# Optimization experiments

Measured on AMD Instinct MI355X. Metric: run time of the kernel, lower is better.

## Reference

```python
import jax, jax.numpy as jnp
import numpy as np

S, B, D, H = 2048, 2, 1024, 16
DK = D // H


def _rope_tables(seq_len, dk):
    inv_freq = 1.0 / (10000.0 ** (np.arange(0, dk, 2, dtype=np.float32) / dk))
    ang = np.arange(seq_len, dtype=np.float32)[:, None] * inv_freq[None, :]  # [S, dk/2]
    ang = np.concatenate([ang, ang], axis=-1)  # [S, dk]
    cos = jnp.asarray(np.cos(ang))[None, None]  # [1,1,S,dk]
    sin = jnp.asarray(np.sin(ang))[None, None]
    return cos, sin


def rotate_half(x):
    x1, x2 = x[..., : x.shape[-1] // 2], x[..., x.shape[-1] // 2 :]
    return jnp.concatenate([-x2, x1], axis=-1)


def apply_rope(x, cos, sin):
    return x * cos + rotate_half(x) * sin


def setup_inputs() -> dict:
    key = jax.random.key(0)
    ks = jax.random.split(key, 12)
    Q = jax.random.normal(ks[0], (S, B, D), dtype=jnp.float32)
    K = jax.random.normal(ks[1], (S, B, D), dtype=jnp.float32)
    V = jax.random.normal(ks[2], (S, B, D), dtype=jnp.float32)
    s = 0.02
    W_q = jax.random.normal(ks[3], (D, D), dtype=jnp.float32) * s
    W_k = jax.random.normal(ks[4], (D, D), dtype=jnp.float32) * s
    W_v = jax.random.normal(ks[5], (D, D), dtype=jnp.float32) * s
    W_o = jax.random.normal(ks[6], (D, D), dtype=jnp.float32) * s
    b_q = jnp.zeros((D,), jnp.float32)
    b_k = jnp.zeros((D,), jnp.float32)
    b_v = jnp.zeros((D,), jnp.float32)
    b_o = jnp.zeros((D,), jnp.float32)
    cos, sin = _rope_tables(S, DK)
    mask = jnp.triu(jnp.ones((S, S), dtype=bool), k=1)[None, None]  # causal, True = masked
    return {
        "Q": Q, "K": K, "V": V,
        "W_q": W_q, "b_q": b_q, "W_k": W_k, "b_k": b_k,
        "W_v": W_v, "b_v": b_v, "W_o": W_o, "b_o": b_o,
        "q_rotary_cos": cos, "q_rotary_sin": sin,
        "k_rotary_cos": cos, "k_rotary_sin": sin,
        "mask": mask,
    }


def reference(Q, K, V, W_q, b_q, W_k, b_k, W_v, b_v, W_o, b_o,
              q_rotary_cos, q_rotary_sin, k_rotary_cos, k_rotary_sin, mask):
    q_len, bsz, _ = Q.shape
    # [S,B,D] -> [S,B,H,dk] -> [B,H,S,dk]
    def proj(x, W, b):
        y = x @ W.T + b
        return y.reshape(x.shape[0], bsz, H, DK).transpose(1, 2, 0, 3)
    q_s = apply_rope(proj(Q, W_q, b_q), q_rotary_cos, q_rotary_sin)
    k_s = apply_rope(proj(K, W_k, b_k), k_rotary_cos, k_rotary_sin)
    v_s = proj(V, W_v, b_v)
    scores = jnp.einsum("bhqd,bhkd->bhqk", q_s, k_s) / jnp.sqrt(jnp.float32(DK))
    scores = jnp.where(mask, jnp.float32(-1e9), scores)
    attn = jax.nn.softmax(scores, axis=-1)
    context = jnp.einsum("bhqk,bhkd->bhqd", attn, v_s)  # [B,H,S,dk]
    context = context.transpose(2, 0, 1, 3).reshape(q_len, bsz, D)
    return context @ W_o.T + b_o
```

## Files before the change

### kernel.cpp

```cpp
#include <hip/hip_runtime.h>
#include <cstdint>
#include <cstddef>

typedef __bf16 bf16;
typedef __bf16 bf16x2 __attribute__((ext_vector_type(2)));
typedef __bf16 bf16x4 __attribute__((ext_vector_type(4)));
typedef __bf16 bf16x8 __attribute__((ext_vector_type(8)));
typedef float f32x4 __attribute__((ext_vector_type(4)));

#define S_LEN 2048
#define BATCH 2
#define DM 1024
#define NH 16
#define DKH 64
#define MTOT (S_LEN * BATCH)

__device__ __forceinline__ void gload_lds16(const void* g, void* l) {
    __builtin_amdgcn_global_load_lds((const __attribute__((address_space(1))) uint32_t*)g,
                                     (__attribute__((address_space(3))) uint32_t*)l, 16, 0, 0);
}

__device__ __forceinline__ uint32_t pack2(float a, float b) {
    bf16x2 v; v[0] = (bf16)a; v[1] = (bf16)b;
    return __builtin_bit_cast(uint32_t, v);
}

struct ConvArgs { const float* src[7]; bf16* dst[7]; };

__global__ __launch_bounds__(256) void convert_all(ConvArgs a) {
    int gid = blockIdx.x * 256 + threadIdx.x;
    int tid, off;
    if (gid < 3 * 524288) { tid = gid >> 19; off = gid & 524287; }
    else { int r = gid - 3 * 524288; tid = 3 + (r >> 17); off = r & 131071; }
    const float4* s4 = (const float4*)a.src[tid];
    float4 x = s4[2 * off], y = s4[2 * off + 1];
    bf16x8 v;
    v[0] = (bf16)x.x; v[1] = (bf16)x.y; v[2] = (bf16)x.z; v[3] = (bf16)x.w;
    v[4] = (bf16)y.x; v[5] = (bf16)y.y; v[6] = (bf16)y.z; v[7] = (bf16)y.w;
    *(bf16x8*)(a.dst[tid] + 8 * (size_t)off) = v;
}

template<int MI>
__device__ __forceinline__ void gemm_core(const bf16* __restrict__ A, const bf16* __restrict__ Bt,
                                          const float* __restrict__ bias, void* __restrict__ out,
                                          int mode, const float* __restrict__ cosp,
                                          const float* __restrict__ sinp, bf16* As, bf16* Bs) {
    constexpr int TN = (MI == 4) ? 128 : 64;
    constexpr int BH = (TN == 128) ? 4096 : 2048;
    const int K = DM;
    int t = threadIdx.x;
    int lane = t & 63, wave = t >> 6;
    int lm = lane & 15, quad = lane >> 4;
    int m0 = blockIdx.y * 128, n0 = blockIdx.x * TN;
    int wm, wn;
    if constexpr (MI == 4) { wm = (wave >> 1) * 64; wn = (wave & 1) * 64; }
    else { wm = wave * 32; wn = 0; }
    f32x4 acc[MI][4] = {};
    int rowg = t >> 2, kc = (t & 3) * 8;
    const bf16* agp0 = A + (size_t)(m0 + rowg) * K + kc;
    const bf16* agp1 = A + (size_t)(m0 + 64 + rowg) * K + kc;
    const bf16* bgp0 = Bt + (size_t)(n0 + rowg) * K + kc;
    const bf16* bgp1 = (TN == 128) ? Bt + (size_t)(n0 + 64 + rowg) * K + kc : nullptr;
    bf16* alds0 = As + wave * 512;
    bf16* alds1 = As + 2048 + wave * 512;
    bf16* blds0 = Bs + wave * 512;
    bf16* blds1 = Bs + 2048 + wave * 512;

    for (int k0 = 0; k0 < K; k0 += 64) {
#pragma unroll
        for (int h = 0; h < 2; ++h) {
            int ko = k0 + h * 32;
            gload_lds16(agp0 + ko, alds0 + h * 4096);
            gload_lds16(agp1 + ko, alds1 + h * 4096);
            gload_lds16(bgp0 + ko, blds0 + h * BH);
            if constexpr (TN == 128) gload_lds16(bgp1 + ko, blds1 + h * BH);
        }
        __syncthreads();
#pragma unroll
        for (int h = 0; h < 2; ++h) {
            bf16x8 af[MI], bfr[4];
#pragma unroll
            for (int i = 0; i < MI; ++i)
                af[i] = *(const bf16x8*)(As + h * 4096 + (wm + i * 16 + lm) * 32 + quad * 8);
#pragma unroll
            for (int j = 0; j < 4; ++j)
                bfr[j] = *(const bf16x8*)(Bs + h * BH + (wn + j * 16 + lm) * 32 + quad * 8);
            if (mode == 1) {
#pragma unroll
                for (int i = 0; i < MI; ++i)
#pragma unroll
                    for (int j = 0; j < 4; ++j)
                        acc[i][j] = __builtin_amdgcn_mfma_f32_16x16x32_bf16(bfr[j], af[i], acc[i][j], 0, 0, 0);
            } else {
#pragma unroll
                for (int i = 0; i < MI; ++i)
#pragma unroll
                    for (int j = 0; j < 4; ++j)
                        acc[i][j] = __builtin_amdgcn_mfma_f32_16x16x32_bf16(af[i], bfr[j], acc[i][j], 0, 0, 0);
            }
        }
        __syncthreads();
    }
    if (mode == 1) {
#pragma unroll
        for (int j = 0; j < 4; ++j) {
#pragma unroll
            for (int r = 0; r < 4; ++r) {
                int d = n0 + wn + j * 16 + quad * 4 + r;
                float bv = bias[d];
                int h = d >> 6, dk = d & 63;
#pragma unroll
                for (int i = 0; i < MI; ++i) {
                    int token = m0 + wm + i * 16 + lm;
                    int s = token >> 1, b = token & 1;
                    ((bf16*)out)[((size_t)(b * NH + h) * DKH + dk) * S_LEN + s] =
                        (bf16)(acc[i][j][r] + bv);
                }
            }
        }
        return;
    }
#pragma unroll
    for (int j = 0; j < 4; ++j) {
        float bcol = bias[n0 + wn + j * 16 + lm];
#pragma unroll
        for (int i = 0; i < MI; ++i)
#pragma unroll
            for (int r = 0; r < 4; ++r) acc[i][j][r] += bcol;
    }
#pragma unroll
    for (int i = 0; i < MI; ++i) {
#pragma unroll
        for (int j = 0; j < 4; ++j) {
            int col = n0 + wn + j * 16 + lm;
#pragma unroll
            for (int r = 0; r < 4; ++r) {
                int row = m0 + wm + i * 16 + quad * 4 + r;
                float val = acc[i][j][r];
                if (mode == 2) {
                    ((float*)out)[(size_t)row * DM + col] = val;
                } else {
                    int s = row >> 1, dk = col & 63;
                    float c = cosp[s * 64 + dk], sn = sinp[s * 64 + dk];
                    float partner = acc[i][j ^ 2][r];
                    float v2 = val * c + (dk < 32 ? -partner : partner) * sn;
                    if (mode == 3) v2 *= 0.125f * 1.44269504088896f;
                    ((bf16*)out)[(size_t)row * DM + col] = (bf16)v2;
                }
            }
        }
    }
}

struct QKVArgs {
    const bf16* A[3]; const bf16* W[3]; const float* bias[3];
    void* out[3]; const float* cs[3]; const float* sn[3]; int mode[3];
};

__global__ __launch_bounds__(256, 2) void gemm_qkv(QKVArgs args) {
    __shared__ __align__(16) bf16 As[8192];
    __shared__ __align__(16) bf16 Bs[8192];
    int z = blockIdx.z;
    gemm_core<4>(args.A[z], args.W[z], args.bias[z], args.out[z], args.mode[z],
                 args.cs[z], args.sn[z], As, Bs);
}

__global__ __launch_bounds__(256, 2) void gemm_one(const bf16* __restrict__ A, const bf16* __restrict__ Bt,
                                                   const float* __restrict__ bias, void* __restrict__ out) {
    __shared__ __align__(16) bf16 As[8192];
    __shared__ __align__(16) bf16 Bs[4096];
    gemm_core<2>(A, Bt, bias, out, 2, nullptr, nullptr, As, Bs);
}

__global__ __launch_bounds__(256, 2) void flash_kernel(const bf16* __restrict__ qp, const bf16* __restrict__ kp,
                                                       const bf16* __restrict__ vT, bf16* __restrict__ ctx) {
    int qta = blockIdx.x;
    int qtb = 31 - qta;
    int bh = blockIdx.y;
    int b = bh >> 4, h = bh & 15;
    int t = threadIdx.x, lane = t & 63, wave = t >> 6;
    int lm = lane & 15, quad = lane >> 4;
    __shared__ __align__(16) bf16 Ks[64 * 64];
    __shared__ __align__(16) bf16 Vs[64 * 64];
    __shared__ __align__(16) uint32_t Pb[4][16 * 37];
    uint32_t* pw = &Pb[wave][0];
    const int q0[2] = {qta * 64 + wave * 16, qtb * 64 + wave * 16};

    bf16x8 aq[2][2];
#pragma unroll
    for (int u = 0; u < 2; ++u) {
        const bf16* qrow = qp + ((size_t)(q0[u] + lm) * BATCH + b) * DM + h * DKH;
        aq[u][0] = *(const bf16x8*)(qrow + quad * 8);
        aq[u][1] = *(const bf16x8*)(qrow + 32 + quad * 8);
    }
    f32x4 o[2][4] = {};
    float l_acc[2] = {0.f, 0.f};

    int r0 = t >> 3, c0 = t & 7;
    int r1 = r0 + 32;
    const bf16* kg0 = kp + ((size_t)r0 * BATCH + b) * DM + h * DKH + c0 * 8;
    const bf16* kg1 = kp + ((size_t)r1 * BATCH + b) * DM + h * DKH + c0 * 8;
    const bf16* vg0 = vT + ((size_t)(bh * DKH + r0)) * S_LEN + c0 * 8;
    const bf16* vg1 = vT + ((size_t)(bh * DKH + r1)) * S_LEN + c0 * 8;
    int lk0 = r0 * 64 + (c0 ^ (r0 & 7)) * 8;
    int lk1 = r1 * 64 + (c0 ^ (r1 & 7)) * 8;
    const size_t kstep = (size_t)64 * BATCH * DM;

    const int niter = qtb + 1;
    bf16x8 ka = *(const bf16x8*)kg0;
    bf16x8 kb2 = *(const bf16x8*)kg1;
    bf16x8 va = *(const bf16x8*)vg0;
    bf16x8 vb2 = *(const bf16x8*)vg1;
    *(bf16x8*)(Ks + lk0) = ka;
    *(bf16x8*)(Ks + lk1) = kb2;
    *(bf16x8*)(Vs + lk0) = va;
    *(bf16x8*)(Vs + lk1) = vb2;
    __syncthreads();

    for (int it = 0; it < niter; ++it) {
        int kv0 = it << 6;
        bool hn = (it + 1) < niter;
        if (hn) {
            size_t koff = (size_t)(it + 1) * kstep;
            ka  = *(const bf16x8*)(kg0 + koff);
            kb2 = *(const bf16x8*)(kg1 + koff);
            va  = *(const bf16x8*)(vg0 + (it + 1) * 64);
            vb2 = *(const bf16x8*)(vg1 + (it + 1) * 64);
        }
        bf16x8 kf[4][2];
#pragma unroll
        for (int nt = 0; nt < 4; ++nt) {
            int krow = nt * 16 + lm;
            kf[nt][0] = *(const bf16x8*)(Ks + krow * 64 + ((quad ^ (krow & 7)) * 8));
            kf[nt][1] = *(const bf16x8*)(Ks + krow * 64 + (((quad + 4) ^ (krow & 7)) * 8));
        }
#pragma unroll
        for (int u = 0; u < 2; ++u) {
            if (u == 0 && kv0 > q0[0] + 15) continue;
            const f32x4 zero = {0.f, 0.f, 0.f, 0.f};
            f32x4 sc[4];
#pragma unroll
            for (int nt = 0; nt < 4; ++nt) {
                sc[nt] = __builtin_amdgcn_mfma_f32_16x16x32_bf16(kf[nt][0], aq[u][0], zero, 0, 0, 0);
                sc[nt] = __builtin_amdgcn_mfma_f32_16x16x32_bf16(kf[nt][1], aq[u][1], sc[nt], 0, 0, 0);
            }
            if (kv0 + 63 > q0[u]) {
#pragma unroll
                for (int nt = 0; nt < 4; ++nt)
#pragma unroll
                    for (int r = 0; r < 4; ++r) {
                        int kvg = kv0 + nt * 16 + quad * 4 + r;
                        if (kvg > q0[u] + lm) sc[nt][r] = -1e30f;
                    }
            }
            float rs = 0.f;
            uint32_t pk[8];
#pragma unroll
            for (int nt = 0; nt < 4; ++nt)
#pragma unroll
                for (int rp = 0; rp < 2; ++rp) {
                    float p0 = exp2f(sc[nt][2 * rp]);
                    float p1 = exp2f(sc[nt][2 * rp + 1]);
                    rs += p0 + p1;
                    pk[nt * 2 + rp] = pack2(p0, p1);
                }
            l_acc[u] += rs;
#pragma unroll
            for (int nt = 0; nt < 4; ++nt)
#pragma unroll
                for (int rp = 0; rp < 2; ++rp)
                    pw[lm * 37 + nt * 8 + quad * 2 + rp] = pk[nt * 2 + rp];
            __builtin_amdgcn_wave_barrier();
            const uint32_t* pr = pw + lm * 37;
            bf16x8 pf0 = *(const bf16x8*)(pr + quad * 4);
            bf16x8 pf1 = *(const bf16x8*)(pr + 16 + quad * 4);
#pragma unroll
            for (int dt = 0; dt < 4; ++dt) {
                int vrow = dt * 16 + lm;
                bf16x8 vf0 = *(const bf16x8*)(Vs + vrow * 64 + ((quad ^ (vrow & 7)) * 8));
                bf16x8 vf1 = *(const bf16x8*)(Vs + vrow * 64 + (((quad + 4) ^ (vrow & 7)) * 8));
                o[u][dt] = __builtin_amdgcn_mfma_f32_16x16x32_bf16(vf0, pf0, o[u][dt], 0, 0, 0);
                o[u][dt] = __builtin_amdgcn_mfma_f32_16x16x32_bf16(vf1, pf1, o[u][dt], 0, 0, 0);
            }
            __builtin_amdgcn_wave_barrier();
        }
        __syncthreads();
        if (hn) {
            *(bf16x8*)(Ks + lk0) = ka;
            *(bf16x8*)(Ks + lk1) = kb2;
            *(bf16x8*)(Vs + lk0) = va;
            *(bf16x8*)(Vs + lk1) = vb2;
        }
        __syncthreads();
    }
#pragma unroll
    for (int u = 0; u < 2; ++u) {
        float l = l_acc[u];
        l += __shfl_xor(l, 16, 64);
        l += __shfl_xor(l, 32, 64);
        float linv = 1.f / l;
        int qg = q0[u] + lm;
        bf16* crow = ctx + ((size_t)qg * BATCH + b) * DM + h * DKH;
#pragma unroll
        for (int dt = 0; dt < 4; ++dt) {
            bf16x4 v;
#pragma unroll
            for (int r = 0; r < 4; ++r) v[r] = (bf16)(o[u][dt][r] * linv);
            *(bf16x4*)(crow + dt * 16 + quad * 4) = v;
        }
    }
}

extern "C" void kernel_launch(void* const* d_in, const int* in_sizes, int n_in,
                              void* d_out, int out_size, void* d_ws, size_t ws_size,
                              hipStream_t stream) {
    const float* Q    = (const float*)d_in[0];
    const float* K    = (const float*)d_in[1];
    const float* V    = (const float*)d_in[2];
    const float* Wq   = (const float*)d_in[3];
    const float* bq   = (const float*)d_in[4];
    const float* Wk   = (const float*)d_in[5];
    const float* bk   = (const float*)d_in[6];
    const float* Wv   = (const float*)d_in[7];
    const float* bv   = (const float*)d_in[8];
    const float* Wo   = (const float*)d_in[9];
    const float* bo   = (const float*)d_in[10];
    const float* qcos = (const float*)d_in[11];
    const float* qsin = (const float*)d_in[12];
    const float* kcos = (const float*)d_in[13];
    const float* ksin = (const float*)d_in[14];

    char* ws = (char*)d_ws;
    const size_t SZ_ACT = (size_t)MTOT * DM * sizeof(bf16);
    const size_t SZ_W   = (size_t)DM * DM * sizeof(bf16);
    bf16* qb  = (bf16*)ws; ws += SZ_ACT;
    bf16* kb  = (bf16*)ws; ws += SZ_ACT;
    bf16* vb  = (bf16*)ws; ws += SZ_ACT;
    bf16* wqb = (bf16*)ws; ws += SZ_W;
    bf16* wkb = (bf16*)ws; ws += SZ_W;
    bf16* wvb = (bf16*)ws; ws += SZ_W;
    bf16* wob = (bf16*)ws; ws += SZ_W;
    bf16* qpr = (bf16*)ws; ws += SZ_ACT;
    bf16* kpr = (bf16*)ws; ws += SZ_ACT;
    bf16* vTp = (bf16*)ws; ws += SZ_ACT;
    bf16* ctx = (bf16*)ws; ws += SZ_ACT;

    ConvArgs ca;
    ca.src[0] = Q;  ca.dst[0] = qb;
    ca.src[1] = K;  ca.dst[1] = kb;
    ca.src[2] = V;  ca.dst[2] = vb;
    ca.src[3] = Wq; ca.dst[3] = wqb;
    ca.src[4] = Wk; ca.dst[4] = wkb;
    ca.src[5] = Wv; ca.dst[5] = wvb;
    ca.src[6] = Wo; ca.dst[6] = wob;
    convert_all<<<8192, 256, 0, stream>>>(ca);

    QKVArgs qa;
    qa.A[0] = qb; qa.W[0] = wqb; qa.bias[0] = bq; qa.out[0] = qpr; qa.mode[0] = 3; qa.cs[0] = qcos; qa.sn[0] = qsin;
    qa.A[1] = kb; qa.W[1] = wkb; qa.bias[1] = bk; qa.out[1] = kpr; qa.mode[1] = 4; qa.cs[1] = kcos; qa.sn[1] = ksin;
    qa.A[2] = vb; qa.W[2] = wvb; qa.bias[2] = bv; qa.out[2] = vTp; qa.mode[2] = 1; qa.cs[2] = nullptr; qa.sn[2] = nullptr;
    gemm_qkv<<<dim3(DM / 128, MTOT / 128, 3), 256, 0, stream>>>(qa);

    flash_kernel<<<dim3(16, BATCH * NH), 256, 0, stream>>>(qpr, kpr, vTp, ctx);

    gemm_one<<<dim3(DM / 64, MTOT / 128), 256, 0, stream>>>(ctx, wob, bo, (float*)d_out);
}
```

Measured before the change: 273.9 us.

## Double-buffer GEMM LDS tiles and swizzle block indices for XCD locality

The projection GEMMs now keep two LDS buffers and issue the global-to-LDS loads for the next K slice before computing on the current one, so memory latency overlaps with MFMA work and one barrier per iteration is removed. Block IDs are also remapped so that blocks running on the same XCD (round-robin by bid mod 8) cover neighbouring tiles, which should improve L2 reuse. LDS use per block doubles, which may limit occupancy under launch_bounds(256,2). The swizzle formulas assume the current grid sizes.

After: 268.4 us. 2.0% less time.

```diff
diff --git a/kernel.cpp b/kernel.cpp
--- a/kernel.cpp
+++ b/kernel.cpp
@@ -44,14 +44,17 @@
 __device__ __forceinline__ void gemm_core(const bf16* __restrict__ A, const bf16* __restrict__ Bt,
                                           const float* __restrict__ bias, void* __restrict__ out,
                                           int mode, const float* __restrict__ cosp,
-                                          const float* __restrict__ sinp, bf16* As, bf16* Bs) {
+                                          const float* __restrict__ sinp, bf16* As, bf16* Bs,
+                                          int bx, int by) {
     constexpr int TN = (MI == 4) ? 128 : 64;
     constexpr int BH = (TN == 128) ? 4096 : 2048;
+    constexpr int ASZ = 8192;
+    constexpr int BSZ = (TN == 128) ? 8192 : 4096;
     const int K = DM;
     int t = threadIdx.x;
     int lane = t & 63, wave = t >> 6;
     int lm = lane & 15, quad = lane >> 4;
-    int m0 = blockIdx.y * 128, n0 = blockIdx.x * TN;
+    int m0 = by * 128, n0 = bx * TN;
     int wm, wn;
     if constexpr (MI == 4) { wm = (wave >> 1) * 64; wn = (wave & 1) * 64; }
     else { wm = wave * 32; wn = 0; }
@@ -61,30 +64,36 @@
     const bf16* agp1 = A + (size_t)(m0 + 64 + rowg) * K + kc;
     const bf16* bgp0 = Bt + (size_t)(n0 + rowg) * K + kc;
     const bf16* bgp1 = (TN == 128) ? Bt + (size_t)(n0 + 64 + rowg) * K + kc : nullptr;
-    bf16* alds0 = As + wave * 512;
-    bf16* alds1 = As + 2048 + wave * 512;
-    bf16* blds0 = Bs + wave * 512;
-    bf16* blds1 = Bs + 2048 + wave * 512;
-
-    for (int k0 = 0; k0 < K; k0 += 64) {
+    int lofs0 = wave * 512;
+    int lofs1 = 2048 + wave * 512;
+
+    auto stage = [&](int k0, bf16* Ab, bf16* Bb) {
 #pragma unroll
         for (int h = 0; h < 2; ++h) {
             int ko = k0 + h * 32;
-            gload_lds16(agp0 + ko, alds0 + h * 4096);
-            gload_lds16(agp1 + ko, alds1 + h * 4096);
-            gload_lds16(bgp0 + ko, blds0 + h * BH);
-            if constexpr (TN == 128) gload_lds16(bgp1 + ko, blds1 + h * BH);
-        }
-        __syncthreads();
+            gload_lds16(agp0 + ko, Ab + lofs0 + h * 4096);
+            gload_lds16(agp1 + ko, Ab + lofs1 + h * 4096);
+            gload_lds16(bgp0 + ko, Bb + lofs0 + h * BH);
+            if constexpr (TN == 128) gload_lds16(bgp1 + ko, Bb + lofs1 + h * BH);
+        }
+    };
+
+    stage(0, As, Bs);
+    __syncthreads();
+    int cur = 0;
+    for (int k0 = 0; k0 < K; k0 += 64) {
+        if (k0 + 64 < K) stage(k0 + 64, As + (cur ^ 1) * ASZ, Bs + (cur ^ 1) * BSZ);
+        const bf16* Ar = As + cur * ASZ;
+        const bf16* Br = Bs + cur * BSZ;
 #pragma unroll
         for (int h = 0; h < 2; ++h) {
             bf16x8 af[MI], bfr[4];
 #pragma unroll
             for (int i = 0; i < MI; ++i)
-                af[i] = *(const bf16x8*)(As + h * 4096 + (wm + i * 16 + lm) * 32 + quad * 8);
+                af[i] = *(const bf16x8*)(Ar + h * 4096 + (wm + i * 16 + lm) * 32 + quad * 8);
 #pragma unroll
             for (int j = 0; j < 4; ++j)
-                bfr[j] = *(const bf16x8*)(Bs + h * BH + (wn + j * 16 + lm) * 32 + quad * 8);
+                bfr[j] = *(const bf16x8*)(Br + h * BH + (wn + j * 16 + lm) * 32 + quad * 8);
             if (mode == 1) {
 #pragma unroll
                 for (int i = 0; i < MI; ++i)
@@ -100,6 +109,7 @@
             }
         }
         __syncthreads();
+        cur ^= 1;
     }
     if (mode == 1) {
 #pragma unroll
@@ -158,18 +168,24 @@
 };
 
 __global__ __launch_bounds__(256, 2) void gemm_qkv(QKVArgs args) {
-    __shared__ __align__(16) bf16 As[8192];
-    __shared__ __align__(16) bf16 Bs[8192];
+    __shared__ __align__(16) bf16 As[2 * 8192];
+    __shared__ __align__(16) bf16 Bs[2 * 8192];
     int z = blockIdx.z;
+    int bid = blockIdx.y * 8 + blockIdx.x;
+    int swz = (bid & 7) * 32 + (bid >> 3);
+    int bx = swz & 7, by = swz >> 3;
     gemm_core<4>(args.A[z], args.W[z], args.bias[z], args.out[z], args.mode[z],
-                 args.cs[z], args.sn[z], As, Bs);
+                 args.cs[z], args.sn[z], As, Bs, bx, by);
 }
 
 __global__ __launch_bounds__(256, 2) void gemm_one(const bf16* __restrict__ A, const bf16* __restrict__ Bt,
                                                    const float* __restrict__ bias, void* __restrict__ out) {
-    __shared__ __align__(16) bf16 As[8192];
-    __shared__ __align__(16) bf16 Bs[4096];
-    gemm_core<2>(A, Bt, bias, out, 2, nullptr, nullptr, As, Bs);
+    __shared__ __align__(16) bf16 As[2 * 8192];
+    __shared__ __align__(16) bf16 Bs[2 * 4096];
+    int bid = blockIdx.y * 16 + blockIdx.x;
+    int swz = (bid & 7) * 64 + (bid >> 3);
+    int bx = swz & 15, by = swz >> 4;
+    gemm_core<2>(A, Bt, bias, out, 2, nullptr, nullptr, As, Bs, bx, by);
 }
 
 __global__ __launch_bounds__(256, 2) void flash_kernel(const bf16* __restrict__ qp, const bf16* __restrict__ kp,
```

## Load GEMM fragments directly from global memory with register double buffering

Applied to the files above, without the earlier changes.

The projection GEMMs stop staging A and B tiles through LDS with global_load_lds and barriers. Each wave now loads its MFMA fragments straight from global memory into registers, double-buffered over K steps of 32, and the launch bounds are raised to 3 blocks per CU. Block indices are swizzled so that consecutively scheduled blocks share L2-resident tiles. This removes LDS traffic and __syncthreads, but duplicates global loads across waves that share rows and uses 16-byte per-lane loads that are only partly coalesced, which puts more pressure on L2 and on registers.

Result: slower. 372.2 us (+35.9%).

```diff
diff --git a/kernel.cpp b/kernel.cpp
--- a/kernel.cpp
+++ b/kernel.cpp
@@ -14,11 +14,6 @@
 #define NH 16
 #define DKH 64
 #define MTOT (S_LEN * BATCH)
-
-__device__ __forceinline__ void gload_lds16(const void* g, void* l) {
-    __builtin_amdgcn_global_load_lds((const __attribute__((address_space(1))) uint32_t*)g,
-                                     (__attribute__((address_space(3))) uint32_t*)l, 16, 0, 0);
-}
 
 __device__ __forceinline__ uint32_t pack2(float a, float b) {
     bf16x2 v; v[0] = (bf16)a; v[1] = (bf16)b;
@@ -44,63 +39,56 @@
 __device__ __forceinline__ void gemm_core(const bf16* __restrict__ A, const bf16* __restrict__ Bt,
                                           const float* __restrict__ bias, void* __restrict__ out,
                                           int mode, const float* __restrict__ cosp,
-                                          const float* __restrict__ sinp, bf16* As, bf16* Bs) {
+                                          const float* __restrict__ sinp, int bx, int by) {
     constexpr int TN = (MI == 4) ? 128 : 64;
-    constexpr int BH = (TN == 128) ? 4096 : 2048;
-    const int K = DM;
+    constexpr int NSTEP = DM / 32;
     int t = threadIdx.x;
     int lane = t & 63, wave = t >> 6;
     int lm = lane & 15, quad = lane >> 4;
-    int m0 = blockIdx.y * 128, n0 = blockIdx.x * TN;
+    int m0 = by * 128, n0 = bx * TN;
     int wm, wn;
     if constexpr (MI == 4) { wm = (wave >> 1) * 64; wn = (wave & 1) * 64; }
     else { wm = wave * 32; wn = 0; }
     f32x4 acc[MI][4] = {};
-    int rowg = t >> 2, kc = (t & 3) * 8;
-    const bf16* agp0 = A + (size_t)(m0 + rowg) * K + kc;
-    const bf16* agp1 = A + (size_t)(m0 + 64 + rowg) * K + kc;
-    const bf16* bgp0 = Bt + (size_t)(n0 + rowg) * K + kc;
-    const bf16* bgp1 = (TN == 128) ? Bt + (size_t)(n0 + 64 + rowg) * K + kc : nullptr;
-    bf16* alds0 = As + wave * 512;
-    bf16* alds1 = As + 2048 + wave * 512;
-    bf16* blds0 = Bs + wave * 512;
-    bf16* blds1 = Bs + 2048 + wave * 512;
-
-    for (int k0 = 0; k0 < K; k0 += 64) {
-#pragma unroll
-        for (int h = 0; h < 2; ++h) {
-            int ko = k0 + h * 32;
-            gload_lds16(agp0 + ko, alds0 + h * 4096);
-            gload_lds16(agp1 + ko, alds1 + h * 4096);
-            gload_lds16(bgp0 + ko, blds0 + h * BH);
-            if constexpr (TN == 128) gload_lds16(bgp1 + ko, blds1 + h * BH);
-        }
-        __syncthreads();
-#pragma unroll
-        for (int h = 0; h < 2; ++h) {
-            bf16x8 af[MI], bfr[4];
+
+    const bf16* pa[MI];
+    const bf16* pb[4];
+#pragma unroll
+    for (int i = 0; i < MI; ++i) pa[i] = A + (size_t)(m0 + wm + i * 16 + lm) * DM + quad * 8;
+#pragma unroll
+    for (int j = 0; j < 4; ++j) pb[j] = Bt + (size_t)(n0 + wn + j * 16 + lm) * DM + quad * 8;
+
+    bf16x8 fa[2][MI], fb[2][4];
+#pragma unroll
+    for (int i = 0; i < MI; ++i) fa[0][i] = *(const bf16x8*)(pa[i]);
+#pragma unroll
+    for (int j = 0; j < 4; ++j) fb[0][j] = *(const bf16x8*)(pb[j]);
+
+#pragma unroll
+    for (int s = 0; s < NSTEP; ++s) {
+        const int cur = s & 1, nxt = cur ^ 1;
+        if (s + 1 < NSTEP) {
+            const int ko = (s + 1) * 32;
+#pragma unroll
+            for (int i = 0; i < MI; ++i) fa[nxt][i] = *(const bf16x8*)(pa[i] + ko);
+#pragma unroll
+            for (int j = 0; j < 4; ++j) fb[nxt][j] = *(const bf16x8*)(pb[j] + ko);
+        }
+        if (mode == 1) {
 #pragma unroll
             for (int i = 0; i < MI; ++i)
-                af[i] = *(const bf16x8*)(As + h * 4096 + (wm + i * 16 + lm) * 32 + quad * 8);
-#pragma unroll
-            for (int j = 0; j < 4; ++j)
-                bfr[j] = *(const bf16x8*)(Bs + h * BH + (wn + j * 16 + lm) * 32 + quad * 8);
-            if (mode == 1) {
-#pragma unroll
-                for (int i = 0; i < MI; ++i)
-#pragma unroll
-                    for (int j = 0; j < 4; ++j)
-                        acc[i][j] = __builtin_amdgcn_mfma_f32_16x16x32_bf16(bfr[j], af[i], acc[i][j], 0, 0, 0);
-            } else {
-#pragma unroll
-                for (int i = 0; i < MI; ++i)
-#pragma unroll
-                    for (int j = 0; j < 4; ++j)
-                        acc[i][j] = __builtin_amdgcn_mfma_f32_16x16x32_bf16(af[i], bfr[j], acc[i][j], 0, 0, 0);
-            }
-        }
-        __syncthreads();
-    }
+#pragma unroll
+                for (int j = 0; j < 4; ++j)
+                    acc[i][j] = __builtin_amdgcn_mfma_f32_16x16x32_bf16(fb[cur][j], fa[cur][i], acc[i][j], 0, 0, 0);
+        } else {
+#pragma unroll
+            for (int i = 0; i < MI; ++i)
+#pragma unroll
+                for (int j = 0; j < 4; ++j)
+                    acc[i][j] = __builtin_amdgcn_mfma_f32_16x16x32_bf16(fa[cur][i], fb[cur][j], acc[i][j], 0, 0, 0);
+        }
+    }
+
     if (mode == 1) {
 #pragma unroll
         for (int j = 0; j < 4; ++j) {
@@ -157,19 +145,21 @@
     void* out[3]; const float* cs[3]; const float* sn[3]; int mode[3];
 };
 
-__global__ __launch_bounds__(256, 2) void gemm_qkv(QKVArgs args) {
-    __shared__ __align__(16) bf16 As[8192];
-    __shared__ __align__(16) bf16 Bs[8192];
+__global__ __launch_bounds__(256, 3) void gemm_qkv(QKVArgs args) {
     int z = blockIdx.z;
+    int bid = blockIdx.y * 8 + blockIdx.x;
+    int swz = (bid & 7) * 32 + (bid >> 3);
+    int bx = swz & 7, by = swz >> 3;
     gemm_core<4>(args.A[z], args.W[z], args.bias[z], args.out[z], args.mode[z],
-                 args.cs[z], args.sn[z], As, Bs);
-}
-
-__global__ __launch_bounds__(256, 2) void gemm_one(const bf16* __restrict__ A, const bf16* __restrict__ Bt,
+                 args.cs[z], args.sn[z], bx, by);
+}
+
+__global__ __launch_bounds__(256, 3) void gemm_one(const bf16* __restrict__ A, const bf16* __restrict__ Bt,
                                                    const float* __restrict__ bias, void* __restrict__ out) {
-    __shared__ __align__(16) bf16 As[8192];
-    __shared__ __align__(16) bf16 Bs[4096];
-    gemm_core<2>(A, Bt, bias, out, 2, nullptr, nullptr, As, Bs);
+    int bid = blockIdx.y * 16 + blockIdx.x;
+    int swz = (bid & 7) * 64 + (bid >> 3);
+    int bx = swz & 15, by = swz >> 4;
+    gemm_core<2>(A, Bt, bias, out, 2, nullptr, nullptr, bx, by);
 }
 
 __global__ __launch_bounds__(256, 2) void flash_kernel(const bf16* __restrict__ qp, const bf16* __restrict__ kp,
```
